# Performance work log

Measured on AMD Instinct MI355X. Metric: run time of the kernel, lower is better.

The kernel has to match this reference:

```python
import jax, jax.numpy as jnp
import numpy as np

CH = 128

def _fir_kernel(ch, factor=2.0):
    # [1,3,3,1] outer product, normalized, scaled by factor**2 (== torch get_fir_kernel)
    k1 = jnp.array([1.0, 3.0, 3.0, 1.0], dtype=jnp.float32)
    k = jnp.outer(k1, k1)
    k = k / k.sum() * (factor ** 2)          # 4x4, sums to 4
    return jnp.tile(k[None, None], (ch, 1, 1, 1))  # (C,1,4,4) OIHW depthwise

def setup_inputs() -> dict:
    key = jax.random.key(0)
    x = jax.random.normal(key, (8, CH, 128, 128), dtype=jnp.float32)
    return {"x": x}

def reference(x) -> jnp.ndarray:
    B, C, H, W = x.shape
    k = _fir_kernel(C, factor=2.0)
    # torch F.conv_transpose2d(x, k, stride=2, padding=1, groups=C)
    # == forward conv with lhs_dilation=2, padding k-1-p=2 each side, spatially flipped kernel
    kf = k[:, :, ::-1, ::-1]  # symmetric kernel, flip for exactness
    out = jax.lax.conv_general_dilated(
        x, kf,
        window_strides=(1, 1),
        padding=((2, 2), (2, 2)),
        lhs_dilation=(2, 2),
        rhs_dilation=(1, 1),
        dimension_numbers=("NCHW", "OIHW", "NCHW"),
        feature_group_count=C,
    )
    # out shape: (B, C, 2H, 2W)
    return out
```

## Files before the change

kernel.cpp:

```cpp
#include <hip/hip_runtime.h>


#define IN_H 128
#define IN_W 128

__global__ __launch_bounds__(256) void upsample_fir_kernel(
    const float* __restrict__ x, float* __restrict__ out) {
    const int tid = threadIdx.x;
    const int lane32 = tid & 31;
    const int r = blockIdx.x * 8 + (tid >> 5);
    const int bc = r >> 7;
    const int iy = r & (IN_H - 1);

    const float* xp = x + (size_t)bc * (IN_H * IN_W);
    const float4 z4 = make_float4(0.f, 0.f, 0.f, 0.f);

    const float4* rowm = (const float4*)(xp + (iy - 1) * IN_W);
    const float4* row0 = (const float4*)(xp + iy * IN_W);
    const float4* rowp = (const float4*)(xp + (iy + 1) * IN_W);

    float4 a = (iy > 0) ? rowm[lane32] : z4;
    float4 b = row0[lane32];
    float4 c = (iy < IN_H - 1) ? rowp[lane32] : z4;

    float4 t, u;
    t.x = (a.x + 3.f * b.x) * 0.25f;  u.x = (3.f * b.x + c.x) * 0.25f;
    t.y = (a.y + 3.f * b.y) * 0.25f;  u.y = (3.f * b.y + c.y) * 0.25f;
    t.z = (a.z + 3.f * b.z) * 0.25f;  u.z = (3.f * b.z + c.z) * 0.25f;
    t.w = (a.w + 3.f * b.w) * 0.25f;  u.w = (3.f * b.w + c.w) * 0.25f;

    float t_l = __shfl_up(t.w, 1);   if (lane32 == 0)  t_l = 0.f;
    float t_r = __shfl_down(t.x, 1); if (lane32 == 31) t_r = 0.f;
    float u_l = __shfl_up(u.w, 1);   if (lane32 == 0)  u_l = 0.f;
    float u_r = __shfl_down(u.x, 1); if (lane32 == 31) u_r = 0.f;

    float4 o0, o1, p0, p1;
    o0.x = (t_l + 3.f * t.x) * 0.25f;
    o0.y = (3.f * t.x + t.y) * 0.25f;
    o0.z = (t.x + 3.f * t.y) * 0.25f;
    o0.w = (3.f * t.y + t.z) * 0.25f;
    o1.x = (t.y + 3.f * t.z) * 0.25f;
    o1.y = (3.f * t.z + t.w) * 0.25f;
    o1.z = (t.z + 3.f * t.w) * 0.25f;
    o1.w = (3.f * t.w + t_r) * 0.25f;

    p0.x = (u_l + 3.f * u.x) * 0.25f;
    p0.y = (3.f * u.x + u.y) * 0.25f;
    p0.z = (u.x + 3.f * u.y) * 0.25f;
    p0.w = (3.f * u.y + u.z) * 0.25f;
    p1.x = (u.y + 3.f * u.z) * 0.25f;
    p1.y = (3.f * u.z + u.w) * 0.25f;
    p1.z = (u.z + 3.f * u.w) * 0.25f;
    p1.w = (3.f * u.w + u_r) * 0.25f;

    const int OW = 2 * IN_W;
    float* ob = out + (size_t)bc * (2 * IN_H) * OW + (size_t)(2 * iy) * OW + 8 * lane32;
    *(float4*)(ob) = o0;
    *(float4*)(ob + 4) = o1;
    *(float4*)(ob + OW) = p0;
    *(float4*)(ob + OW + 4) = p1;
}

extern "C" void kernel_launch(void* const* d_in, const int* in_sizes, int n_in,
                              void* d_out, int out_size, void* d_ws, size_t ws_size,
                              hipStream_t stream) {
    const float* x = (const float*)d_in[0];
    float* out = (float*)d_out;
    int blocks = (8 * 128 * 128) / 8;
    upsample_fir_kernel<<<blocks, 256, 0, stream>>>(x, out);
}
```

Before: 334.0 us.

## Stream rows per wave with rolling window to reuse input rows

Each 64-lane wave now processes 16 consecutive input rows of one channel. It keeps the previous and current rows in registers and loads only the next row each iteration, instead of reloading three rows per output row. Lanes handle float2 input and write float4 output across full 64-wide waves, and the grid becomes one 512-thread block per channel. This cuts redundant global reads but serialises each wave's work over a row loop, which lowers parallelism and latency hiding per wave.

```diff
diff --git a/kernel.cpp b/kernel.cpp
--- a/kernel.cpp
+++ b/kernel.cpp
@@ -3,62 +3,57 @@
 
 #define IN_H 128
 #define IN_W 128
+#define ROWS_PER_WAVE 16
 
-__global__ __launch_bounds__(256) void upsample_fir_kernel(
+__global__ __launch_bounds__(512) void upsample_fir_kernel(
     const float* __restrict__ x, float* __restrict__ out) {
-    const int tid = threadIdx.x;
-    const int lane32 = tid & 31;
-    const int r = blockIdx.x * 8 + (tid >> 5);
-    const int bc = r >> 7;
-    const int iy = r & (IN_H - 1);
+    const int lane = threadIdx.x & 63;
+    const int wv   = threadIdx.x >> 6;
+    const int bc   = blockIdx.x;
+    const int iy0  = wv * ROWS_PER_WAVE;
 
     const float* xp = x + (size_t)bc * (IN_H * IN_W);
-    const float4 z4 = make_float4(0.f, 0.f, 0.f, 0.f);
+    const int OW = 2 * IN_W;
+    float* op = out + (size_t)bc * (2 * IN_H) * OW + 4 * lane;
 
-    const float4* rowm = (const float4*)(xp + (iy - 1) * IN_W);
-    const float4* row0 = (const float4*)(xp + iy * IN_W);
-    const float4* rowp = (const float4*)(xp + (iy + 1) * IN_W);
+    const float2 z2 = make_float2(0.f, 0.f);
 
-    float4 a = (iy > 0) ? rowm[lane32] : z4;
-    float4 b = row0[lane32];
-    float4 c = (iy < IN_H - 1) ? rowp[lane32] : z4;
+    float2 a = (iy0 > 0) ? ((const float2*)(xp + (iy0 - 1) * IN_W))[lane] : z2;
+    float2 b = ((const float2*)(xp + iy0 * IN_W))[lane];
 
-    float4 t, u;
-    t.x = (a.x + 3.f * b.x) * 0.25f;  u.x = (3.f * b.x + c.x) * 0.25f;
-    t.y = (a.y + 3.f * b.y) * 0.25f;  u.y = (3.f * b.y + c.y) * 0.25f;
-    t.z = (a.z + 3.f * b.z) * 0.25f;  u.z = (3.f * b.z + c.z) * 0.25f;
-    t.w = (a.w + 3.f * b.w) * 0.25f;  u.w = (3.f * b.w + c.w) * 0.25f;
+    #pragma unroll 4
+    for (int iy = iy0; iy < iy0 + ROWS_PER_WAVE; ++iy) {
+        const int ny = (iy + 1 < IN_H) ? (iy + 1) : (IN_H - 1);
+        float2 cr = ((const float2*)(xp + ny * IN_W))[lane];
+        float2 c;
+        c.x = (iy + 1 < IN_H) ? cr.x : 0.f;
+        c.y = (iy + 1 < IN_H) ? cr.y : 0.f;
 
-    float t_l = __shfl_up(t.w, 1);   if (lane32 == 0)  t_l = 0.f;
-    float t_r = __shfl_down(t.x, 1); if (lane32 == 31) t_r = 0.f;
-    float u_l = __shfl_up(u.w, 1);   if (lane32 == 0)  u_l = 0.f;
-    float u_r = __shfl_down(u.x, 1); if (lane32 == 31) u_r = 0.f;
+        float2 t, u;
+        t.x = (a.x + 3.f * b.x) * 0.25f;  u.x = (3.f * b.x + c.x) * 0.25f;
+        t.y = (a.y + 3.f * b.y) * 0.25f;  u.y = (3.f * b.y + c.y) * 0.25f;
 
-    float4 o0, o1, p0, p1;
-    o0.x = (t_l + 3.f * t.x) * 0.25f;
-    o0.y = (3.f * t.x + t.y) * 0.25f;
-    o0.z = (t.x + 3.f * t.y) * 0.25f;
-    o0.w = (3.f * t.y + t.z) * 0.25f;
-    o1.x = (t.y + 3.f * t.z) * 0.25f;
-    o1.y = (3.f * t.z + t.w) * 0.25f;
-    o1.z = (t.z + 3.f * t.w) * 0.25f;
-    o1.w = (3.f * t.w + t_r) * 0.25f;
+        float t_l = __shfl_up(t.y, 1);   if (lane == 0)  t_l = 0.f;
+        float t_r = __shfl_down(t.x, 1); if (lane == 63) t_r = 0.f;
+        float u_l = __shfl_up(u.y, 1);   if (lane == 0)  u_l = 0.f;
+        float u_r = __shfl_down(u.x, 1); if (lane == 63) u_r = 0.f;
 
-    p0.x = (u_l + 3.f * u.x) * 0.25f;
-    p0.y = (3.f * u.x + u.y) * 0.25f;
-    p0.z = (u.x + 3.f * u.y) * 0.25f;
-    p0.w = (3.f * u.y + u.z) * 0.25f;
-    p1.x = (u.y + 3.f * u.z) * 0.25f;
-    p1.y = (3.f * u.z + u.w) * 0.25f;
-    p1.z = (u.z + 3.f * u.w) * 0.25f;
-    p1.w = (3.f * u.w + u_r) * 0.25f;
+        float4 o, p;
+        o.x = (t_l + 3.f * t.x) * 0.25f;
+        o.y = (3.f * t.x + t.y) * 0.25f;
+        o.z = (t.x + 3.f * t.y) * 0.25f;
+        o.w = (3.f * t.y + t_r) * 0.25f;
+        p.x = (u_l + 3.f * u.x) * 0.25f;
+        p.y = (3.f * u.x + u.y) * 0.25f;
+        p.z = (u.x + 3.f * u.y) * 0.25f;
+        p.w = (3.f * u.y + u_r) * 0.25f;
 
-    const int OW = 2 * IN_W;
-    float* ob = out + (size_t)bc * (2 * IN_H) * OW + (size_t)(2 * iy) * OW + 8 * lane32;
-    *(float4*)(ob) = o0;
-    *(float4*)(ob + 4) = o1;
-    *(float4*)(ob + OW) = p0;
-    *(float4*)(ob + OW + 4) = p1;
+        float* ob = op + (size_t)(2 * iy) * OW;
+        *(float4*)(ob)      = o;
+        *(float4*)(ob + OW) = p;
+
+        a = b; b = c;
+    }
 }
 
 extern "C" void kernel_launch(void* const* d_in, const int* in_sizes, int n_in,
@@ -66,6 +61,5 @@
                               hipStream_t stream) {
     const float* x = (const float*)d_in[0];
     float* out = (float*)d_out;
-    int blocks = (8 * 128 * 128) / 8;
-    upsample_fir_kernel<<<blocks, 256, 0, stream>>>(x, out);
+    upsample_fir_kernel<<<8 * 128, 512, 0, stream>>>(x, out);
 }
```

Measured after the change: 314.4 us. -5.9%, faster.
